# Optimization experiments

Hardware: AMD Instinct MI355X
Metric: run time of the kernel (lower is better)

## Reference

```python
import jax, jax.numpy as jnp
import numpy as np

B, D_IN, T = 16, 512, 4096
D_CB, K = 8, 1024
COMMITMENT = 1.0


def _weight_norm(v, g):
    # torch weight_norm with dim=0: w[o] = g[o] * v[o] / ||v[o]||
    return g[:, None] * v / jnp.sqrt(jnp.sum(v * v, axis=1, keepdims=True))


def setup_inputs() -> dict:
    key = jax.random.key(0)
    ks = jax.random.split(key, 8)
    return {
        "z": jax.random.normal(ks[0], (B, D_IN, T), dtype=jnp.float32),
        "in_v": jax.random.normal(ks[1], (D_CB, D_IN), dtype=jnp.float32) * 0.05,
        "in_g": jax.random.uniform(ks[2], (D_CB,), dtype=jnp.float32, minval=0.5, maxval=1.5),
        "in_b": jax.random.normal(ks[3], (D_CB,), dtype=jnp.float32) * 0.01,
        "out_v": jax.random.normal(ks[4], (D_IN, D_CB), dtype=jnp.float32) * 0.05,
        "out_g": jax.random.uniform(ks[5], (D_IN,), dtype=jnp.float32, minval=0.5, maxval=1.5),
        "out_b": jax.random.normal(ks[6], (D_IN,), dtype=jnp.float32) * 0.01,
        "codebook": jax.random.normal(ks[7], (K, D_CB), dtype=jnp.float32),
    }


def reference(z, in_v, in_g, in_b, out_v, out_g, out_b, codebook):
    z = z.astype(jnp.float32)
    # in_project: weight-normed 1x1 conv == per-timestep linear [D_IN -> D_CB]
    w_in = _weight_norm(in_v, in_g)                       # [D_CB, D_IN]
    z_e = jnp.einsum('cd,bdt->bct', w_in, z) + in_b[None, :, None]  # [B, D_CB, T]

    enc = jnp.transpose(z_e, (0, 2, 1))                   # [B, T, D_CB]
    cb = codebook.astype(jnp.float32)                     # [K, D_CB]
    # squared euclidean distance via expansion
    d = (jnp.sum(enc * enc, axis=-1, keepdims=True)
         - 2.0 * jnp.einsum('btd,kd->btk', enc, cb)
         + jnp.sum(cb * cb, axis=-1)[None, None, :])      # [B, T, K]
    indices = jnp.argmin(d, axis=-1)                      # [B, T] int

    z_q = jnp.transpose(cb[indices], (0, 2, 1))           # [B, D_CB, T]
    commit_loss = jnp.mean((z_e - jax.lax.stop_gradient(z_q)) ** 2, axis=(1, 2)) * COMMITMENT  # [B]

    # straight-through estimator
    z_q_st = z_e + jax.lax.stop_gradient(z_q - z_e)

    w_out = _weight_norm(out_v, out_g)                    # [D_IN, D_CB]
    out = jnp.einsum('cd,bdt->bct', w_out, z_q_st) + out_b[None, :, None]  # [B, D_IN, T]
    return out, commit_loss, indices
```

## Files before the change

kernel.cpp:

```cpp
#include <hip/hip_runtime.h>
#include <math.h>

#define NB 16
#define DIN 512
#define TT 4096
#define DCB 8
#define KC 1024
#define NW 8


__global__ __launch_bounds__(512) void vq_setup(
    const float* __restrict__ in_v, const float* __restrict__ in_g,
    const float* __restrict__ out_v, const float* __restrict__ out_g,
    const float* __restrict__ cb, float* __restrict__ ws)
{
    int tid = threadIdx.x;
    float* w_inT = ws;
    float* w_out = ws + 4096;
    float* cb2   = ws + 8192;

    {
        int c    = tid >> 6;
        int lane = tid & 63;
        const float* v = in_v + c * DIN;
        float s = 0.f;
        #pragma unroll
        for (int i = 0; i < DIN; i += 64) {
            float x = v[i + lane];
            s += x * x;
        }
        #pragma unroll
        for (int off = 32; off > 0; off >>= 1) s += __shfl_xor(s, off, 64);
        float sq = sqrtf(s);
        float g  = in_g[c];
        #pragma unroll
        for (int i = 0; i < DIN; i += 64) {
            int d = i + lane;
            w_inT[d * DCB + c] = (g * v[d]) / sq;
        }
    }
    {
        int o = tid;
        const float* v = out_v + o * DCB;
        float s = 0.f;
        #pragma unroll
        for (int c = 0; c < DCB; ++c) s += v[c] * v[c];
        float sq = sqrtf(s);
        float g  = out_g[o];
        #pragma unroll
        for (int c = 0; c < DCB; ++c) w_out[o * DCB + c] = (g * v[c]) / sq;
    }
    for (int k = tid; k < KC; k += 512) {
        const float* r = cb + k * DCB;
        float s = 0.f;
        #pragma unroll
        for (int c = 0; c < DCB; ++c) s += r[c] * r[c];
        cb2[k] = s;
    }
}

__global__ __launch_bounds__(512, 8) void vq_main(
    const float* __restrict__ z, const float* __restrict__ in_b,
    const float* __restrict__ out_b, const float* __restrict__ cb,
    const float* __restrict__ ws, float* __restrict__ ws_commit,
    float* __restrict__ out)
{
    __shared__ float s_buf[KC * DCB];
    __shared__ float s_sd[NW][64];
    __shared__ int   s_si[NW][64];

    const float* w_inT = ws;
    const float* w_out = ws + 4096;
    const float* cb2w  = ws + 8192;

    int tid  = threadIdx.x;
    int w    = tid >> 6;
    int wu   = __builtin_amdgcn_readfirstlane(w);
    int lane = tid & 63;
    int blk  = blockIdx.x;
    int b    = blk >> 6;
    int t    = (blk & 63) * 64 + lane;

    const float* zp = z + (size_t)b * DIN * TT + t;

    float ze[DCB];
    #pragma unroll
    for (int c = 0; c < DCB; ++c) ze[c] = 0.f;

    int d0 = wu * 64;
    #pragma unroll 4
    for (int dd = 0; dd < 64; ++dd) {
        int d = d0 + dd;
        float zv = zp[(size_t)d * TT];
        const float* wi = w_inT + d * DCB;
        #pragma unroll
        for (int c = 0; c < DCB; ++c) ze[c] = fmaf(wi[c], zv, ze[c]);
    }

    float* redw = s_buf + w * (DCB * 64);
    #pragma unroll
    for (int c = 0; c < DCB; ++c) redw[c * 64 + lane] = ze[c];

    float4 p0 = ((const float4*)cb)[tid];
    float4 p1 = ((const float4*)cb)[512 + tid];
    float4 p2 = ((const float4*)cb)[1024 + tid];
    float4 p3 = ((const float4*)cb)[1536 + tid];

    __syncthreads();

    #pragma unroll
    for (int c = 0; c < DCB; ++c) {
        float s = 0.f;
        #pragma unroll
        for (int w2 = 0; w2 < NW; ++w2) s += s_buf[w2 * (DCB * 64) + c * 64 + lane];
        ze[c] = s + in_b[c];
    }
    __syncthreads();

    ((float4*)s_buf)[tid]        = p0;
    ((float4*)s_buf)[512 + tid]  = p1;
    ((float4*)s_buf)[1024 + tid] = p2;
    ((float4*)s_buf)[1536 + tid] = p3;
    __syncthreads();

    float enc2 = 0.f;
    #pragma unroll
    for (int c = 0; c < DCB; ++c) enc2 += ze[c] * ze[c];

    float best = 3.4e38f;
    int   bi   = 0;
    int   k0   = wu * 128;
    #pragma unroll 4
    for (int kk = 0; kk < 128; ++kk) {
        int k = k0 + kk;
        float4 r0 = ((const float4*)s_buf)[2 * k];
        float4 r1 = ((const float4*)s_buf)[2 * k + 1];
        float dot = fmaf(ze[0], r0.x, fmaf(ze[1], r0.y, fmaf(ze[2], r0.z, fmaf(ze[3], r0.w,
                    fmaf(ze[4], r1.x, fmaf(ze[5], r1.y, fmaf(ze[6], r1.z, ze[7] * r1.w)))))));
        float dk  = (enc2 - 2.0f * dot) + cb2w[k];
        if (dk < best) { best = dk; bi = k; }
    }
    s_sd[w][lane] = best;
    s_si[w][lane] = bi;
    __syncthreads();

    float gbest = s_sd[0][lane];
    int   gbi   = s_si[0][lane];
    #pragma unroll
    for (int w2 = 1; w2 < NW; ++w2) {
        float d2 = s_sd[w2][lane];
        int   i2 = s_si[w2][lane];
        if (d2 < gbest) { gbest = d2; gbi = i2; }
    }

    float4 qa = ((const float4*)s_buf)[2 * gbi];
    float4 qb = ((const float4*)s_buf)[2 * gbi + 1];

    if (wu == 0) {
        float cl = 0.f, f;
        f = ze[0]-qa.x; cl = fmaf(f,f,cl);
        f = ze[1]-qa.y; cl = fmaf(f,f,cl);
        f = ze[2]-qa.z; cl = fmaf(f,f,cl);
        f = ze[3]-qa.w; cl = fmaf(f,f,cl);
        f = ze[4]-qb.x; cl = fmaf(f,f,cl);
        f = ze[5]-qb.y; cl = fmaf(f,f,cl);
        f = ze[6]-qb.z; cl = fmaf(f,f,cl);
        f = ze[7]-qb.w; cl = fmaf(f,f,cl);
        #pragma unroll
        for (int off = 32; off > 0; off >>= 1) cl += __shfl_xor(cl, off, 64);
        if (lane == 0) ws_commit[blk] = cl;
        out[(size_t)NB * DIN * TT + NB + (size_t)b * TT + t] = (float)gbi;
    }

    float* outp = out + (size_t)b * DIN * TT + t;
    int o0 = wu * 64;
    #pragma unroll 4
    for (int oo = 0; oo < 64; ++oo) {
        int o = o0 + oo;
        const float* wo = w_out + o * DCB;
        float obias = out_b[o];
        float a = fmaf(wo[0], qa.x, fmaf(wo[1], qa.y, fmaf(wo[2], qa.z, fmaf(wo[3], qa.w,
                  fmaf(wo[4], qb.x, fmaf(wo[5], qb.y, fmaf(wo[6], qb.z, wo[7] * qb.w)))))));
        outp[(size_t)o * TT] = a + obias;
    }
}

__global__ __launch_bounds__(64) void vq_commit(
    const float* __restrict__ ws_commit, float* __restrict__ out)
{
    int b    = blockIdx.x;
    int lane = threadIdx.x;
    float s = ws_commit[b * 64 + lane];
    #pragma unroll
    for (int off = 32; off > 0; off >>= 1) s += __shfl_xor(s, off, 64);
    if (lane == 0)
        out[(size_t)NB * DIN * TT + b] = s * (1.0f / (DCB * TT));
}

extern "C" void kernel_launch(void* const* d_in, const int* in_sizes, int n_in,
                              void* d_out, int out_size, void* d_ws, size_t ws_size,
                              hipStream_t stream) {
    const float* z     = (const float*)d_in[0];
    const float* in_v  = (const float*)d_in[1];
    const float* in_g  = (const float*)d_in[2];
    const float* in_b  = (const float*)d_in[3];
    const float* out_v = (const float*)d_in[4];
    const float* out_g = (const float*)d_in[5];
    const float* out_b = (const float*)d_in[6];
    const float* cb    = (const float*)d_in[7];

    float* ws  = (float*)d_ws;
    float* out = (float*)d_out;

    vq_setup<<<1, 512, 0, stream>>>(in_v, in_g, out_v, out_g, cb, ws);
    vq_main<<<1024, 512, 0, stream>>>(z, in_b, out_b, cb, ws, ws + 9216, out);
    vq_commit<<<NB, 64, 0, stream>>>(ws + 9216, out);
}
```

Baseline: 71.78 us.

## Process two time tiles per block, overlapping second tile's z loads with first output stores

Each block now handles two 64-timestep tiles, halving the grid to 512 blocks. The codebook is loaded into shared memory once per block and reused by both tiles. The second tile's z reads are interleaved with the first tile's output writes, so load and store traffic overlap. The cost is extra shared memory (separate reduction buffers per tile), lower launch-bounds occupancy and fewer blocks to spread across CUs.

```diff
diff --git a/kernel.cpp b/kernel.cpp
--- a/kernel.cpp
+++ b/kernel.cpp
@@ -59,15 +59,19 @@
     }
 }
 
-__global__ __launch_bounds__(512, 8) void vq_main(
+__global__ __launch_bounds__(512, 4) void vq_main(
     const float* __restrict__ z, const float* __restrict__ in_b,
     const float* __restrict__ out_b, const float* __restrict__ cb,
     const float* __restrict__ ws, float* __restrict__ ws_commit,
     float* __restrict__ out)
 {
-    __shared__ float s_buf[KC * DCB];
-    __shared__ float s_sd[NW][64];
-    __shared__ int   s_si[NW][64];
+    __shared__ float s_cb[KC * DCB];
+    __shared__ float s_redA[NW * DCB * 64];
+    __shared__ float s_redB[NW * DCB * 64];
+    __shared__ float s_sdA[NW][64];
+    __shared__ int   s_siA[NW][64];
+    __shared__ float s_sdB[NW][64];
+    __shared__ int   s_siB[NW][64];
 
     const float* w_inT = ws;
     const float* w_out = ws + 4096;
@@ -78,110 +82,198 @@
     int wu   = __builtin_amdgcn_readfirstlane(w);
     int lane = tid & 63;
     int blk  = blockIdx.x;
-    int b    = blk >> 6;
-    int t    = (blk & 63) * 64 + lane;
-
-    const float* zp = z + (size_t)b * DIN * TT + t;
-
-    float ze[DCB];
-    #pragma unroll
-    for (int c = 0; c < DCB; ++c) ze[c] = 0.f;
-
+    int b    = blk >> 5;
+    int p    = blk & 31;
+    int tA   = p * 128 + lane;
+
+    {
+        float4 c0 = ((const float4*)cb)[tid];
+        float4 c1 = ((const float4*)cb)[512 + tid];
+        float4 c2 = ((const float4*)cb)[1024 + tid];
+        float4 c3 = ((const float4*)cb)[1536 + tid];
+        ((float4*)s_cb)[tid]        = c0;
+        ((float4*)s_cb)[512 + tid]  = c1;
+        ((float4*)s_cb)[1024 + tid] = c2;
+        ((float4*)s_cb)[1536 + tid] = c3;
+    }
+
+    const float* zpA = z + (size_t)b * DIN * TT + tA;
     int d0 = wu * 64;
-    #pragma unroll 4
-    for (int dd = 0; dd < 64; ++dd) {
-        int d = d0 + dd;
-        float zv = zp[(size_t)d * TT];
-        const float* wi = w_inT + d * DCB;
-        #pragma unroll
-        for (int c = 0; c < DCB; ++c) ze[c] = fmaf(wi[c], zv, ze[c]);
-    }
-
-    float* redw = s_buf + w * (DCB * 64);
-    #pragma unroll
-    for (int c = 0; c < DCB; ++c) redw[c * 64 + lane] = ze[c];
-
-    float4 p0 = ((const float4*)cb)[tid];
-    float4 p1 = ((const float4*)cb)[512 + tid];
-    float4 p2 = ((const float4*)cb)[1024 + tid];
-    float4 p3 = ((const float4*)cb)[1536 + tid];
-
+
+    float zeA[DCB];
+    #pragma unroll
+    for (int c = 0; c < DCB; ++c) zeA[c] = 0.f;
+    for (int db = 0; db < 64; db += 8) {
+        float v[8];
+        #pragma unroll
+        for (int j = 0; j < 8; ++j) v[j] = zpA[(size_t)(d0 + db + j) * TT];
+        #pragma unroll
+        for (int j = 0; j < 8; ++j) {
+            const float* wi = w_inT + (d0 + db + j) * DCB;
+            #pragma unroll
+            for (int c = 0; c < DCB; ++c) zeA[c] = fmaf(wi[c], v[j], zeA[c]);
+        }
+    }
+    {
+        float* redw = s_redA + w * (DCB * 64);
+        #pragma unroll
+        for (int c = 0; c < DCB; ++c) redw[c * 64 + lane] = zeA[c];
+    }
     __syncthreads();
 
     #pragma unroll
     for (int c = 0; c < DCB; ++c) {
         float s = 0.f;
         #pragma unroll
-        for (int w2 = 0; w2 < NW; ++w2) s += s_buf[w2 * (DCB * 64) + c * 64 + lane];
-        ze[c] = s + in_b[c];
+        for (int w2 = 0; w2 < NW; ++w2) s += s_redA[w2 * (DCB * 64) + c * 64 + lane];
+        zeA[c] = s + in_b[c];
+    }
+
+    float enc2 = 0.f;
+    #pragma unroll
+    for (int c = 0; c < DCB; ++c) enc2 += zeA[c] * zeA[c];
+    {
+        float best = 3.4e38f;
+        int   bi   = 0;
+        int   k0   = wu * 128;
+        #pragma unroll 4
+        for (int kk = 0; kk < 128; ++kk) {
+            int k = k0 + kk;
+            float4 r0 = ((const float4*)s_cb)[2 * k];
+            float4 r1 = ((const float4*)s_cb)[2 * k + 1];
+            float dot = fmaf(zeA[0], r0.x, fmaf(zeA[1], r0.y, fmaf(zeA[2], r0.z, fmaf(zeA[3], r0.w,
+                        fmaf(zeA[4], r1.x, fmaf(zeA[5], r1.y, fmaf(zeA[6], r1.z, zeA[7] * r1.w)))))));
+            float dk  = (enc2 - 2.0f * dot) + cb2w[k];
+            if (dk < best) { best = dk; bi = k; }
+        }
+        s_sdA[w][lane] = best;
+        s_siA[w][lane] = bi;
     }
     __syncthreads();
 
-    ((float4*)s_buf)[tid]        = p0;
-    ((float4*)s_buf)[512 + tid]  = p1;
-    ((float4*)s_buf)[1024 + tid] = p2;
-    ((float4*)s_buf)[1536 + tid] = p3;
-    __syncthreads();
-
-    float enc2 = 0.f;
-    #pragma unroll
-    for (int c = 0; c < DCB; ++c) enc2 += ze[c] * ze[c];
-
-    float best = 3.4e38f;
-    int   bi   = 0;
-    int   k0   = wu * 128;
-    #pragma unroll 4
-    for (int kk = 0; kk < 128; ++kk) {
-        int k = k0 + kk;
-        float4 r0 = ((const float4*)s_buf)[2 * k];
-        float4 r1 = ((const float4*)s_buf)[2 * k + 1];
-        float dot = fmaf(ze[0], r0.x, fmaf(ze[1], r0.y, fmaf(ze[2], r0.z, fmaf(ze[3], r0.w,
-                    fmaf(ze[4], r1.x, fmaf(ze[5], r1.y, fmaf(ze[6], r1.z, ze[7] * r1.w)))))));
-        float dk  = (enc2 - 2.0f * dot) + cb2w[k];
-        if (dk < best) { best = dk; bi = k; }
-    }
-    s_sd[w][lane] = best;
-    s_si[w][lane] = bi;
-    __syncthreads();
-
-    float gbest = s_sd[0][lane];
-    int   gbi   = s_si[0][lane];
+    float gbest = s_sdA[0][lane];
+    int   gbiA  = s_siA[0][lane];
     #pragma unroll
     for (int w2 = 1; w2 < NW; ++w2) {
-        float d2 = s_sd[w2][lane];
-        int   i2 = s_si[w2][lane];
-        if (d2 < gbest) { gbest = d2; gbi = i2; }
-    }
-
-    float4 qa = ((const float4*)s_buf)[2 * gbi];
-    float4 qb = ((const float4*)s_buf)[2 * gbi + 1];
+        float d2 = s_sdA[w2][lane];
+        int   i2 = s_siA[w2][lane];
+        if (d2 < gbest) { gbest = d2; gbiA = i2; }
+    }
+    float4 qAa = ((const float4*)s_cb)[2 * gbiA];
+    float4 qAb = ((const float4*)s_cb)[2 * gbiA + 1];
 
     if (wu == 0) {
         float cl = 0.f, f;
-        f = ze[0]-qa.x; cl = fmaf(f,f,cl);
-        f = ze[1]-qa.y; cl = fmaf(f,f,cl);
-        f = ze[2]-qa.z; cl = fmaf(f,f,cl);
-        f = ze[3]-qa.w; cl = fmaf(f,f,cl);
-        f = ze[4]-qb.x; cl = fmaf(f,f,cl);
-        f = ze[5]-qb.y; cl = fmaf(f,f,cl);
-        f = ze[6]-qb.z; cl = fmaf(f,f,cl);
-        f = ze[7]-qb.w; cl = fmaf(f,f,cl);
+        f = zeA[0]-qAa.x; cl = fmaf(f,f,cl);
+        f = zeA[1]-qAa.y; cl = fmaf(f,f,cl);
+        f = zeA[2]-qAa.z; cl = fmaf(f,f,cl);
+        f = zeA[3]-qAa.w; cl = fmaf(f,f,cl);
+        f = zeA[4]-qAb.x; cl = fmaf(f,f,cl);
+        f = zeA[5]-qAb.y; cl = fmaf(f,f,cl);
+        f = zeA[6]-qAb.z; cl = fmaf(f,f,cl);
+        f = zeA[7]-qAb.w; cl = fmaf(f,f,cl);
         #pragma unroll
         for (int off = 32; off > 0; off >>= 1) cl += __shfl_xor(cl, off, 64);
-        if (lane == 0) ws_commit[blk] = cl;
-        out[(size_t)NB * DIN * TT + NB + (size_t)b * TT + t] = (float)gbi;
-    }
-
-    float* outp = out + (size_t)b * DIN * TT + t;
-    int o0 = wu * 64;
+        if (lane == 0) ws_commit[b * 64 + 2 * p] = cl;
+        out[(size_t)NB * DIN * TT + NB + (size_t)b * TT + tA] = (float)gbiA;
+    }
+
+    const float* zpB  = zpA + 64;
+    float* outpA = out + (size_t)b * DIN * TT + tA;
+    float zeB[DCB];
+    #pragma unroll
+    for (int c = 0; c < DCB; ++c) zeB[c] = 0.f;
+    for (int i = 0; i < 64; i += 4) {
+        float v[4];
+        #pragma unroll
+        for (int j = 0; j < 4; ++j) v[j] = zpB[(size_t)(d0 + i + j) * TT];
+        #pragma unroll
+        for (int j = 0; j < 4; ++j) {
+            int o = d0 + i + j;
+            const float* wo = w_out + o * DCB;
+            float a = fmaf(wo[0], qAa.x, fmaf(wo[1], qAa.y, fmaf(wo[2], qAa.z, fmaf(wo[3], qAa.w,
+                      fmaf(wo[4], qAb.x, fmaf(wo[5], qAb.y, fmaf(wo[6], qAb.z, wo[7] * qAb.w)))))));
+            outpA[(size_t)o * TT] = a + out_b[o];
+        }
+        #pragma unroll
+        for (int j = 0; j < 4; ++j) {
+            const float* wi = w_inT + (d0 + i + j) * DCB;
+            #pragma unroll
+            for (int c = 0; c < DCB; ++c) zeB[c] = fmaf(wi[c], v[j], zeB[c]);
+        }
+    }
+    {
+        float* redw = s_redB + w * (DCB * 64);
+        #pragma unroll
+        for (int c = 0; c < DCB; ++c) redw[c * 64 + lane] = zeB[c];
+    }
+    __syncthreads();
+
+    #pragma unroll
+    for (int c = 0; c < DCB; ++c) {
+        float s = 0.f;
+        #pragma unroll
+        for (int w2 = 0; w2 < NW; ++w2) s += s_redB[w2 * (DCB * 64) + c * 64 + lane];
+        zeB[c] = s + in_b[c];
+    }
+
+    float enc2b = 0.f;
+    #pragma unroll
+    for (int c = 0; c < DCB; ++c) enc2b += zeB[c] * zeB[c];
+    {
+        float best = 3.4e38f;
+        int   bi   = 0;
+        int   k0   = wu * 128;
+        #pragma unroll 4
+        for (int kk = 0; kk < 128; ++kk) {
+            int k = k0 + kk;
+            float4 r0 = ((const float4*)s_cb)[2 * k];
+            float4 r1 = ((const float4*)s_cb)[2 * k + 1];
+            float dot = fmaf(zeB[0], r0.x, fmaf(zeB[1], r0.y, fmaf(zeB[2], r0.z, fmaf(zeB[3], r0.w,
+                        fmaf(zeB[4], r1.x, fmaf(zeB[5], r1.y, fmaf(zeB[6], r1.z, zeB[7] * r1.w)))))));
+            float dk  = (enc2b - 2.0f * dot) + cb2w[k];
+            if (dk < best) { best = dk; bi = k; }
+        }
+        s_sdB[w][lane] = best;
+        s_siB[w][lane] = bi;
+    }
+    __syncthreads();
+
+    float gbestB = s_sdB[0][lane];
+    int   gbiB   = s_siB[0][lane];
+    #pragma unroll
+    for (int w2 = 1; w2 < NW; ++w2) {
+        float d2 = s_sdB[w2][lane];
+        int   i2 = s_siB[w2][lane];
+        if (d2 < gbestB) { gbestB = d2; gbiB = i2; }
+    }
+    float4 qBa = ((const float4*)s_cb)[2 * gbiB];
+    float4 qBb = ((const float4*)s_cb)[2 * gbiB + 1];
+
+    if (wu == 0) {
+        float cl = 0.f, f;
+        f = zeB[0]-qBa.x; cl = fmaf(f,f,cl);
+        f = zeB[1]-qBa.y; cl = fmaf(f,f,cl);
+        f = zeB[2]-qBa.z; cl = fmaf(f,f,cl);
+        f = zeB[3]-qBa.w; cl = fmaf(f,f,cl);
+        f = zeB[4]-qBb.x; cl = fmaf(f,f,cl);
+        f = zeB[5]-qBb.y; cl = fmaf(f,f,cl);
+        f = zeB[6]-qBb.z; cl = fmaf(f,f,cl);
+        f = zeB[7]-qBb.w; cl = fmaf(f,f,cl);
+        #pragma unroll
+        for (int off = 32; off > 0; off >>= 1) cl += __shfl_xor(cl, off, 64);
+        if (lane == 0) ws_commit[b * 64 + 2 * p + 1] = cl;
+        out[(size_t)NB * DIN * TT + NB + (size_t)b * TT + tA + 64] = (float)gbiB;
+    }
+
+    float* outpB = outpA + 64;
     #pragma unroll 4
     for (int oo = 0; oo < 64; ++oo) {
-        int o = o0 + oo;
+        int o = d0 + oo;
         const float* wo = w_out + o * DCB;
-        float obias = out_b[o];
-        float a = fmaf(wo[0], qa.x, fmaf(wo[1], qa.y, fmaf(wo[2], qa.z, fmaf(wo[3], qa.w,
-                  fmaf(wo[4], qb.x, fmaf(wo[5], qb.y, fmaf(wo[6], qb.z, wo[7] * qb.w)))))));
-        outp[(size_t)o * TT] = a + obias;
+        float a = fmaf(wo[0], qBa.x, fmaf(wo[1], qBa.y, fmaf(wo[2], qBa.z, fmaf(wo[3], qBa.w,
+                  fmaf(wo[4], qBb.x, fmaf(wo[5], qBb.y, fmaf(wo[6], qBb.z, wo[7] * qBb.w)))))));
+        outpB[(size_t)o * TT] = a + out_b[o];
     }
 }
 
@@ -213,6 +305,6 @@
     float* out = (float*)d_out;
 
     vq_setup<<<1, 512, 0, stream>>>(in_v, in_g, out_v, out_g, cb, ws);
-    vq_main<<<1024, 512, 0, stream>>>(z, in_b, out_b, cb, ws, ws + 9216, out);
+    vq_main<<<512, 512, 0, stream>>>(z, in_b, out_b, cb, ws, ws + 9216, out);
     vq_commit<<<NB, 64, 0, stream>>>(ws + 9216, out);
 }
```

Measured after the change: 76.66 us. 1.07x slower.
